# Performance work log

Hardware: AMD Instinct MI355X
Metric: run time of the kernel (lower is better)

## Reference

```python
import jax, jax.numpy as jnp
import numpy as np

B, L, H, HD = 2, 2048, 16, 64
C = H * HD
POS_DIM = 1
MIN_FREQ, MAX_FREQ, P_ZERO = 0.5, 40.0, 0.0


def _phi(m):
    # generalized golden ratio (root of x**(m+1) = x + 1)
    x = 2.0
    for _ in range(100):
        x = (1.0 + x) ** (1.0 / (m + 1))
    return x


def _make_rope_freqs():
    """Golden-gate RoPE frequencies: (H, HD//2, POS_DIM).
    Log-spaced magnitudes in [min_freq, max_freq] (times 2*pi), quasi-random
    unit directions in pos_dim space; leading p_zero_freqs fraction zeroed."""
    n_freqs = HD // 2
    total = H * n_freqs
    n_zero = int(round(total * P_ZERO))
    n_nz = total - n_zero
    mags = MIN_FREQ * (MAX_FREQ / MIN_FREQ) ** (np.arange(n_nz) / max(n_nz - 1, 1))
    mags = np.concatenate([np.zeros(n_zero), mags]) * (2.0 * np.pi)
    if POS_DIM == 1:
        dirs = np.ones((total, 1), dtype=np.float64)
    else:
        g = _phi(POS_DIM)
        alpha = (1.0 / g) ** np.arange(1, POS_DIM + 1)
        z = np.modf(np.arange(1, total + 1)[:, None] * alpha)[0]
        z = np.clip(z, 1e-6, 1 - 1e-6)
        dirs = np.asarray(jax.scipy.special.ndtri(jnp.asarray(z)))
        dirs = dirs / np.linalg.norm(dirs, axis=-1, keepdims=True)
    freqs = dirs * mags[:, None]
    return jnp.asarray(freqs.reshape(H, n_freqs, POS_DIM), dtype=jnp.float32)


def setup_inputs() -> dict:
    key = jax.random.key(0)
    k_x, k_qkv, k_out = jax.random.split(key, 3)
    x = jax.random.normal(k_x, (B, L, C), dtype=jnp.float32)
    w_qkv = jax.random.normal(k_qkv, (C, 3 * C), dtype=jnp.float32) / np.sqrt(C)
    b_qkv = jnp.zeros((3 * C,), dtype=jnp.float32)
    w_out = jax.random.normal(k_out, (C, C), dtype=jnp.float32) / np.sqrt(C)
    b_out = jnp.zeros((C,), dtype=jnp.float32)
    rope_freqs = _make_rope_freqs()
    return {"x": x, "w_qkv": w_qkv, "b_qkv": b_qkv, "w_out": w_out,
            "b_out": b_out, "rope_freqs": rope_freqs}


def _forward(x, w_qkv, b_qkv, w_out, b_out, rope_freqs):
    b, l, c = x.shape
    qkv = x @ w_qkv + b_qkv                                   # (b,l,3c)
    qkv = qkv.reshape(b, l, 3, H, HD).transpose(0, 3, 1, 2, 4)  # (b,h,l,3,hd)
    q, k, v = qkv[..., 0, :], qkv[..., 1, :], qkv[..., 2, :]   # (b,h,l,hd)
    # positions: arange, pos_dim = 1 -> (b,l,1)
    pos = jnp.broadcast_to(jnp.arange(l, dtype=jnp.float32)[None, :, None], (b, l, POS_DIM))
    theta = jnp.einsum('blp,hfp->blhf', pos, rope_freqs)       # (b,l,h,hd/2)
    cos, sin = jnp.cos(theta), jnp.sin(theta)

    def rot(t):  # t: (b,h,l,hd) -> rotate half-split pairs
        t = t.transpose(0, 2, 1, 3)                            # (b,l,h,hd)
        t1, t2 = jnp.split(t, 2, axis=-1)
        r = jnp.concatenate([t1 * cos - t2 * sin, t1 * sin + t2 * cos], axis=-1)
        return r.transpose(0, 2, 1, 3)                         # (b,h,l,hd)

    q_rot, k_rot = rot(q), rot(k)
    logits = jnp.einsum('bhld,bhmd->bhlm', q_rot, k_rot) / jnp.sqrt(jnp.float32(HD))
    attn = jax.nn.softmax(logits, axis=-1)
    out = jnp.einsum('bhlm,bhmd->bhld', attn, v)
    out = out.transpose(0, 2, 1, 3).reshape(b, l, H * HD)
    return out @ w_out + b_out


def reference(x, w_qkv, b_qkv, w_out, b_out, rope_freqs):
    return _forward(x, w_qkv, b_qkv, w_out, b_out, rope_freqs)
```

## Files before the change

### kernel.cpp

```cpp
#include <hip/hip_runtime.h>
#include <cstddef>
#include <cstdint>


typedef __attribute__((ext_vector_type(8))) short short8;
typedef __attribute__((ext_vector_type(4))) float f32x4;
typedef __attribute__((ext_vector_type(4))) unsigned short ushort4_t;
typedef __attribute__((ext_vector_type(2))) unsigned int uint2_t;

__device__ __forceinline__ unsigned short f2bf(float f) {
  union { float f; unsigned int u; } c{f};
  unsigned int u = c.u;
  u += 0x7fff + ((u >> 16) & 1);
  return (unsigned short)(u >> 16);
}
__device__ __forceinline__ float bf2f(unsigned short h) {
  union { unsigned int u; float f; } c{((unsigned int)h) << 16};
  return c.f;
}
__device__ __forceinline__ unsigned int pack_bf16_trunc(float a, float b) {
  union { float f; unsigned int u; } ca{a}, cb{b};
  return __builtin_amdgcn_perm(cb.u, ca.u, 0x07060302u);
}

__global__ __launch_bounds__(256) void cvt_f32_bf16(const float* __restrict__ src,
                                                    unsigned short* __restrict__ dst,
                                                    int n4) {
  int i = blockIdx.x * 256 + threadIdx.x;
  int stride = gridDim.x * 256;
  for (; i < n4; i += stride) {
    float4 v = reinterpret_cast<const float4*>(src)[i];
    ushort4_t o;
    o.x = f2bf(v.x); o.y = f2bf(v.y); o.z = f2bf(v.z); o.w = f2bf(v.w);
    reinterpret_cast<ushort4_t*>(dst)[i] = o;
  }
}

__global__ __launch_bounds__(256) void transpose_cvt(const float* __restrict__ W,
                                                     unsigned short* __restrict__ WT,
                                                     int K, int N) {
  __shared__ float T[64][65];
  const int n0 = blockIdx.x * 64, k0 = blockIdx.y * 64;
  const int t = threadIdx.x;
  const int r = t >> 4, c4 = (t & 15) * 4;
#pragma unroll
  for (int rr = 0; rr < 4; ++rr) {
    int kk = rr * 16 + r;
    float4 v = *reinterpret_cast<const float4*>(W + (size_t)(k0 + kk) * N + n0 + c4);
    T[kk][c4 + 0] = v.x; T[kk][c4 + 1] = v.y; T[kk][c4 + 2] = v.z; T[kk][c4 + 3] = v.w;
  }
  __syncthreads();
#pragma unroll
  for (int rr = 0; rr < 4; ++rr) {
    int nn = rr * 16 + r;
    ushort4_t o;
    o.x = f2bf(T[c4 + 0][nn]); o.y = f2bf(T[c4 + 1][nn]);
    o.z = f2bf(T[c4 + 2][nn]); o.w = f2bf(T[c4 + 3][nn]);
    *reinterpret_cast<ushort4_t*>(WT + (size_t)(n0 + nn) * K + k0 + c4) = o;
  }
}

template <int EPI>
__global__ __launch_bounds__(256) void mm128p(const unsigned short* __restrict__ A,
                                              const unsigned short* __restrict__ Bt,
                                              const float* __restrict__ bias,
                                              unsigned short* __restrict__ q,
                                              unsigned short* __restrict__ k,
                                              unsigned short* __restrict__ v,
                                              float* __restrict__ outf) {
  __shared__ unsigned short As[128][40];
  __shared__ unsigned short Bs[128][40];
  const int m0 = blockIdx.y * 128, n0 = blockIdx.x * 128;
  const int t = threadIdx.x, l = t & 63, w = t >> 6;
  const int wm = w >> 1, wn = w & 1;
  const int lr = l & 15, lg = l >> 4;
  const int lrow = t >> 1, lk = (t & 1) * 16;

  const unsigned short* ap = A + (size_t)(m0 + lrow) * 1024 + lk;
  const unsigned short* bp = Bt + (size_t)(n0 + lrow) * 1024 + lk;

  short8 av0 = *reinterpret_cast<const short8*>(ap);
  short8 av1 = *reinterpret_cast<const short8*>(ap + 8);
  short8 bv0 = *reinterpret_cast<const short8*>(bp);
  short8 bv1 = *reinterpret_cast<const short8*>(bp + 8);

  f32x4 acc[4][4] = {};
#pragma unroll 2
  for (int k0 = 0; k0 < 1024; k0 += 32) {
    __syncthreads();
    *reinterpret_cast<short8*>(&As[lrow][lk]) = av0;
    *reinterpret_cast<short8*>(&As[lrow][lk + 8]) = av1;
    *reinterpret_cast<short8*>(&Bs[lrow][lk]) = bv0;
    *reinterpret_cast<short8*>(&Bs[lrow][lk + 8]) = bv1;
    __syncthreads();
    const int kn = (k0 + 32) & 1023;
    short8 an0 = *reinterpret_cast<const short8*>(ap + kn);
    short8 an1 = *reinterpret_cast<const short8*>(ap + kn + 8);
    short8 bn0 = *reinterpret_cast<const short8*>(bp + kn);
    short8 bn1 = *reinterpret_cast<const short8*>(bp + kn + 8);
    short8 af[4], bf[4];
#pragma unroll
    for (int i = 0; i < 4; ++i)
      af[i] = *reinterpret_cast<const short8*>(&As[wm * 64 + i * 16 + lr][lg * 8]);
#pragma unroll
    for (int j = 0; j < 4; ++j)
      bf[j] = *reinterpret_cast<const short8*>(&Bs[wn * 64 + j * 16 + lr][lg * 8]);
#pragma unroll
    for (int i = 0; i < 4; ++i)
#pragma unroll
      for (int j = 0; j < 4; ++j)
        acc[i][j] = __builtin_amdgcn_mfma_f32_16x16x32_bf16(af[i], bf[j], acc[i][j], 0, 0, 0);
    av0 = an0; av1 = an1; bv0 = bn0; bv1 = bn1;
  }

  if constexpr (EPI == 0) {
#pragma unroll
    for (int j = 0; j < 4; ++j) {
      const int n = n0 + wn * 64 + j * 16 + lr;
      const float bb = bias[n];
      const int s = n >> 10, cc = n & 1023, h = cc >> 6, d = cc & 63;
      unsigned short* dst = (s == 0) ? q : (s == 1) ? k : v;
#pragma unroll
      for (int i = 0; i < 4; ++i)
#pragma unroll
        for (int r = 0; r < 4; ++r) {
          const int m = m0 + wm * 64 + i * 16 + lg * 4 + r;
          const int b = m >> 11, lseq = m & 2047;
          dst[(size_t)(((b << 4) + h) * 2048 + lseq) * 64 + d] = f2bf(acc[i][j][r] + bb);
        }
    }
  } else {
#pragma unroll
    for (int j = 0; j < 4; ++j) {
      const int n = n0 + wn * 64 + j * 16 + lr;
      const float bb = bias[n];
#pragma unroll
      for (int i = 0; i < 4; ++i)
#pragma unroll
        for (int r = 0; r < 4; ++r) {
          const int m = m0 + wm * 64 + i * 16 + lg * 4 + r;
          outf[(size_t)m * 1024 + n] = acc[i][j][r] + bb;
        }
    }
  }
}

__global__ __launch_bounds__(256) void rope_bf(unsigned short* __restrict__ q,
                                               unsigned short* __restrict__ k,
                                               const float* __restrict__ freqs) {
  const int tid = blockIdx.x * 256 + threadIdx.x;
  const int f = tid & 31, row = tid >> 5;
  const int lseq = row & 2047, h = (row >> 11) & 15;
  const float th = (float)lseq * freqs[h * 32 + f];
  float s, c;
  sincosf(th, &s, &c);
  const float QS = 0.18033688011112042f;
  unsigned short* qp = q + (size_t)row * 64;
  const float q1 = bf2f(qp[f]), q2 = bf2f(qp[f + 32]);
  qp[f]      = f2bf((q1 * c - q2 * s) * QS);
  qp[f + 32] = f2bf((q1 * s + q2 * c) * QS);
  unsigned short* kp = k + (size_t)row * 64;
  const float k1 = bf2f(kp[f]), k2 = bf2f(kp[f + 32]);
  kp[f]      = f2bf(k1 * c - k2 * s);
  kp[f + 32] = f2bf(k1 * s + k2 * c);
}

__global__ __launch_bounds__(256) void transpose_v(const unsigned short* __restrict__ V,
                                                   unsigned short* __restrict__ Vt) {
  __shared__ unsigned short T[64][72];
  const int bh = blockIdx.y, l0 = blockIdx.x * 64;
  const int t = threadIdx.x;
  const int r = t >> 2, c16 = (t & 3) * 16;
  const unsigned short* src = V + (size_t)bh * 2048 * 64 + (size_t)(l0 + r) * 64 + c16;
  *reinterpret_cast<short8*>(&T[r][c16])     = *reinterpret_cast<const short8*>(src);
  *reinterpret_cast<short8*>(&T[r][c16 + 8]) = *reinterpret_cast<const short8*>(src + 8);
  __syncthreads();
  short8 o0, o1;
#pragma unroll
  for (int jj = 0; jj < 8; ++jj) o0[jj] = (short)T[c16 + jj][r];
#pragma unroll
  for (int jj = 0; jj < 8; ++jj) o1[jj] = (short)T[c16 + 8 + jj][r];
  unsigned short* dst = Vt + ((size_t)bh * 64 + r) * 2048 + l0 + c16;
  *reinterpret_cast<short8*>(dst) = o0;
  *reinterpret_cast<short8*>(dst + 8) = o1;
}

__global__ __launch_bounds__(256, 2) void attn_mfma5(const unsigned short* __restrict__ Q,
                                                     const unsigned short* __restrict__ K,
                                                     const unsigned short* __restrict__ Vt,
                                                     unsigned short* __restrict__ O) {
  __shared__ unsigned short Ks[2][64 * 64];
  __shared__ unsigned short Vs[2][64 * 64];
  __shared__ unsigned short Pb[4][4][16][72];
  const int bh = blockIdx.y, q0 = blockIdx.x * 256;
  const int t = threadIdx.x, l = t & 63, w = t >> 6;
  const int lr = l & 15, lg = l >> 4;
  const unsigned short* Qb = Q + (size_t)bh * (2048 * 64);
  const unsigned short* Kb = K + (size_t)bh * (2048 * 64);
  const unsigned short* Vb = Vt + (size_t)bh * (64 * 2048);
  const int qrow = q0 + w * 64;

  const int srow = w * 16 + (l >> 3);
  const int xo   = ((l & 7) ^ (srow & 7)) * 8;
  const int swzA = srow * 64 + xo;
  const int swzB = (srow + 8) * 64 + xo;
  const unsigned short* kgp = Kb + (size_t)srow * 64 + (l & 7) * 8;
  const unsigned short* vgp = Vb + (size_t)srow * 2048 + (l & 7) * 8;

  short8 qf[4][2];
#pragma unroll
  for (int g = 0; g < 4; ++g)
#pragma unroll
    for (int h = 0; h < 2; ++h)
      qf[g][h] = *reinterpret_cast<const short8*>(Qb + (size_t)(qrow + g * 16 + lr) * 64 + h * 32 + lg * 8);

  f32x4 oacc[4][4] = {};
  float m_run[4] = {-3.0e38f, -3.0e38f, -3.0e38f, -3.0e38f};
  float l_run[4] = {0.0f, 0.0f, 0.0f, 0.0f};

  {
    short8 k0a = *reinterpret_cast<const short8*>(kgp);
    short8 k0b = *reinterpret_cast<const short8*>(kgp + 8 * 64);
    short8 v0a = *reinterpret_cast<const short8*>(vgp);
    short8 v0b = *reinterpret_cast<const short8*>(vgp + 8 * 2048);
    *reinterpret_cast<short8*>(&Ks[0][swzA]) = k0a;
    *reinterpret_cast<short8*>(&Ks[0][swzB]) = k0b;
    *reinterpret_cast<short8*>(&Vs[0][swzA]) = v0a;
    *reinterpret_cast<short8*>(&Vs[0][swzB]) = v0b;
  }

  for (int it = 0; it < 32; ++it) {
    const int cur = it & 1;
    __syncthreads();

    short8 kna, knb, vna, vnb;
    if (it < 31) {
      kna = *reinterpret_cast<const short8*>(kgp + (size_t)(it + 1) * 4096);
      knb = *reinterpret_cast<const short8*>(kgp + (size_t)(it + 1) * 4096 + 8 * 64);
      vna = *reinterpret_cast<const short8*>(vgp + (it + 1) * 64);
      vnb = *reinterpret_cast<const short8*>(vgp + (it + 1) * 64 + 8 * 2048);
    }

    short8 kfa[4][2];
#pragma unroll
    for (int n = 0; n < 4; ++n)
#pragma unroll
      for (int h = 0; h < 2; ++h)
        kfa[n][h] = *reinterpret_cast<const short8*>(
            &Ks[cur][(n * 16 + lr) * 64 + (((h * 4 + lg) ^ (lr & 7)) * 8)]);

#pragma unroll
    for (int g = 0; g < 4; ++g) {
      f32x4 sacc[4] = {};
      __builtin_amdgcn_s_setprio(1);
#pragma unroll
      for (int n = 0; n < 4; ++n) {
        sacc[n] = __builtin_amdgcn_mfma_f32_16x16x32_bf16(kfa[n][0], qf[g][0], sacc[n], 0, 0, 0);
        sacc[n] = __builtin_amdgcn_mfma_f32_16x16x32_bf16(kfa[n][1], qf[g][1], sacc[n], 0, 0, 0);
      }
      __builtin_amdgcn_s_setprio(0);
      float m0 = fmaxf(fmaxf(sacc[0][0], sacc[0][1]), fmaxf(sacc[0][2], sacc[0][3]));
      float m1 = fmaxf(fmaxf(sacc[1][0], sacc[1][1]), fmaxf(sacc[1][2], sacc[1][3]));
      float m2 = fmaxf(fmaxf(sacc[2][0], sacc[2][1]), fmaxf(sacc[2][2], sacc[2][3]));
      float m3 = fmaxf(fmaxf(sacc[3][0], sacc[3][1]), fmaxf(sacc[3][2], sacc[3][3]));
      float mx = fmaxf(fmaxf(m0, m1), fmaxf(m2, m3));
      mx = fmaxf(mx, __shfl_xor(mx, 16));
      mx = fmaxf(mx, __shfl_xor(mx, 32));
      if (__any(mx > m_run[g] + 8.0f)) {
        const float m_new = fmaxf(m_run[g], mx);
        const float alpha = __builtin_amdgcn_exp2f(m_run[g] - m_new);
        m_run[g] = m_new;
        l_run[g] *= alpha;
#pragma unroll
        for (int sub = 0; sub < 4; ++sub)
#pragma unroll
          for (int r = 0; r < 4; ++r) oacc[g][sub][r] *= alpha;
      }
      const float mq = m_run[g];
      float p[16];
#pragma unroll
      for (int n = 0; n < 4; ++n)
#pragma unroll
        for (int r = 0; r < 4; ++r)
          p[n * 4 + r] = __builtin_amdgcn_exp2f(sacc[n][r] - mq);
      float ssum = ((p[0] + p[1]) + (p[2] + p[3])) + ((p[4] + p[5]) + (p[6] + p[7]));
      ssum += ((p[8] + p[9]) + (p[10] + p[11])) + ((p[12] + p[13]) + (p[14] + p[15]));
      ssum += __shfl_xor(ssum, 16);
      ssum += __shfl_xor(ssum, 32);
      l_run[g] += ssum;
#pragma unroll
      for (int n = 0; n < 4; ++n) {
        uint2_t pk;
        pk.x = pack_bf16_trunc(p[n * 4 + 0], p[n * 4 + 1]);
        pk.y = pack_bf16_trunc(p[n * 4 + 2], p[n * 4 + 3]);
        *reinterpret_cast<uint2_t*>(&Pb[w][g][lr][n * 16 + lg * 4]) = pk;
      }
    }

    short8 vfa[4][2];
#pragma unroll
    for (int sub = 0; sub < 4; ++sub)
#pragma unroll
      for (int kb = 0; kb < 2; ++kb)
        vfa[sub][kb] = *reinterpret_cast<const short8*>(
            &Vs[cur][(sub * 16 + lr) * 64 + (((kb * 4 + lg) ^ (lr & 7)) * 8)]);

#pragma unroll
    for (int g = 0; g < 4; ++g) {
      short8 pb[2];
#pragma unroll
      for (int kb = 0; kb < 2; ++kb)
        pb[kb] = *reinterpret_cast<const short8*>(&Pb[w][g][lr][kb * 32 + lg * 8]);
      __builtin_amdgcn_s_setprio(1);
#pragma unroll
      for (int sub = 0; sub < 4; ++sub) {
        oacc[g][sub] = __builtin_amdgcn_mfma_f32_16x16x32_bf16(vfa[sub][0], pb[0], oacc[g][sub], 0, 0, 0);
        oacc[g][sub] = __builtin_amdgcn_mfma_f32_16x16x32_bf16(vfa[sub][1], pb[1], oacc[g][sub], 0, 0, 0);
      }
      __builtin_amdgcn_s_setprio(0);
    }

    __syncthreads();
    if (it < 31) {
      const int nxt = cur ^ 1;
      *reinterpret_cast<short8*>(&Ks[nxt][swzA]) = kna;
      *reinterpret_cast<short8*>(&Ks[nxt][swzB]) = knb;
      *reinterpret_cast<short8*>(&Vs[nxt][swzA]) = vna;
      *reinterpret_cast<short8*>(&Vs[nxt][swzB]) = vnb;
    }
  }

  const int b = bh >> 4, h = bh & 15;
#pragma unroll
  for (int g = 0; g < 4; ++g) {
    const float inv = 1.0f / l_run[g];
    unsigned short* Ob = O + ((size_t)(b * 2048 + qrow + g * 16 + lr)) * 1024 + h * 64;
#pragma unroll
    for (int sub = 0; sub < 4; ++sub) {
      ushort4_t o;
#pragma unroll
      for (int r = 0; r < 4; ++r) o[r] = f2bf(oacc[g][sub][r] * inv);
      *reinterpret_cast<ushort4_t*>(Ob + sub * 16 + lg * 4) = o;
    }
  }
}

extern "C" void kernel_launch(void* const* d_in, const int* in_sizes, int n_in,
                              void* d_out, int out_size, void* d_ws, size_t ws_size,
                              hipStream_t stream) {
  const float* x          = (const float*)d_in[0];
  const float* w_qkv      = (const float*)d_in[1];
  const float* b_qkv      = (const float*)d_in[2];
  const float* w_out      = (const float*)d_in[3];
  const float* b_out      = (const float*)d_in[4];
  const float* rope_freqs = (const float*)d_in[5];
  float* out = (float*)d_out;

  char* ws = (char*)d_ws;
  unsigned short* x_bf    = (unsigned short*)(ws + 0);
  unsigned short* attn_bf = x_bf;
  unsigned short* q_bf    = (unsigned short*)(ws + 8388608);
  unsigned short* k_bf    = (unsigned short*)(ws + 16777216);
  unsigned short* v_bf    = (unsigned short*)(ws + 25165824);
  unsigned short* v_t     = (unsigned short*)(ws + 33554432);
  unsigned short* wqkvT   = (unsigned short*)(ws + 41943040);
  unsigned short* woutT   = (unsigned short*)(ws + 48234496);

  hipLaunchKernelGGL(cvt_f32_bf16, dim3(1024), dim3(256), 0, stream, x, x_bf, 1048576);
  hipLaunchKernelGGL(transpose_cvt, dim3(48, 16), dim3(256), 0, stream, w_qkv, wqkvT, 1024, 3072);
  hipLaunchKernelGGL(transpose_cvt, dim3(16, 16), dim3(256), 0, stream, w_out, woutT, 1024, 1024);
  hipLaunchKernelGGL((mm128p<0>), dim3(24, 32), dim3(256), 0, stream,
                     x_bf, wqkvT, b_qkv, q_bf, k_bf, v_bf, (float*)nullptr);
  hipLaunchKernelGGL(rope_bf, dim3(8192), dim3(256), 0, stream, q_bf, k_bf, rope_freqs);
  hipLaunchKernelGGL(transpose_v, dim3(32, 32), dim3(256), 0, stream, v_bf, v_t);
  hipLaunchKernelGGL(attn_mfma5, dim3(8, 32), dim3(256), 0, stream, q_bf, k_bf, v_t, attn_bf);
  hipLaunchKernelGGL((mm128p<1>), dim3(8, 32), dim3(256), 0, stream,
                     attn_bf, woutT, b_out,
                     (unsigned short*)nullptr, (unsigned short*)nullptr, (unsigned short*)nullptr, out);
}
```

Measured before the change: 256.6 us.

## Fuse RoPE and V transpose into QKV GEMM epilogue, remap blocks per XCD

The QKV GEMM epilogue now applies bias, RoPE (with the q scale folded in) and writes V directly in transposed layout. This removes the separate rope_bf and transpose_v kernels along with their extra global memory round trips. It also switches the GEMM and attention grids to 1D and remaps block indices so blocks sharing data land on the same XCD, aiming for better L2 reuse. The cost is more sincos work inside the GEMM epilogue and strided scalar stores for q and k.

```diff
diff --git a/kernel.cpp b/kernel.cpp
--- a/kernel.cpp
+++ b/kernel.cpp
@@ -60,17 +60,21 @@
   }
 }
 
-template <int EPI>
+template <int EPI, int NPX>
 __global__ __launch_bounds__(256) void mm128p(const unsigned short* __restrict__ A,
                                               const unsigned short* __restrict__ Bt,
                                               const float* __restrict__ bias,
                                               unsigned short* __restrict__ q,
                                               unsigned short* __restrict__ k,
                                               unsigned short* __restrict__ v,
-                                              float* __restrict__ outf) {
+                                              float* __restrict__ outf,
+                                              const float* __restrict__ freqs) {
   __shared__ unsigned short As[128][40];
   __shared__ unsigned short Bs[128][40];
-  const int m0 = blockIdx.y * 128, n0 = blockIdx.x * 128;
+  const int bid = blockIdx.x;
+  const int xcd = bid & 7, c = bid >> 3;
+  const int m0 = (c & 31) * 128;
+  const int n0 = (xcd * NPX + (c >> 5)) * 128;
   const int t = threadIdx.x, l = t & 63, w = t >> 6;
   const int wm = w >> 1, wn = w & 1;
   const int lr = l & 15, lg = l >> 4;
@@ -114,20 +118,51 @@
   }
 
   if constexpr (EPI == 0) {
-#pragma unroll
-    for (int j = 0; j < 4; ++j) {
-      const int n = n0 + wn * 64 + j * 16 + lr;
-      const float bb = bias[n];
-      const int s = n >> 10, cc = n & 1023, h = cc >> 6, d = cc & 63;
-      unsigned short* dst = (s == 0) ? q : (s == 1) ? k : v;
+    const int nbase = n0 + wn * 64;
+    const int s = nbase >> 10;
+    const int h = (nbase >> 6) & 15;
+    const float b0 = bias[nbase + lr],      b1 = bias[nbase + 16 + lr];
+    const float b2 = bias[nbase + 32 + lr], b3 = bias[nbase + 48 + lr];
+    if (s < 2) {
+      unsigned short* dst = (s == 0) ? q : k;
+      const float scale = (s == 0) ? 0.18033688011112042f : 1.0f;
+      const float f0 = freqs[h * 32 + lr];
+      const float f1 = freqs[h * 32 + 16 + lr];
 #pragma unroll
       for (int i = 0; i < 4; ++i)
 #pragma unroll
         for (int r = 0; r < 4; ++r) {
           const int m = m0 + wm * 64 + i * 16 + lg * 4 + r;
-          const int b = m >> 11, lseq = m & 2047;
-          dst[(size_t)(((b << 4) + h) * 2048 + lseq) * 64 + d] = f2bf(acc[i][j][r] + bb);
+          const int bb = m >> 11, lseq = m & 2047;
+          float sn0, cs0, sn1, cs1;
+          sincosf((float)lseq * f0, &sn0, &cs0);
+          sincosf((float)lseq * f1, &sn1, &cs1);
+          const float t0 = acc[i][0][r] + b0;
+          const float t1 = acc[i][1][r] + b1;
+          const float t2 = acc[i][2][r] + b2;
+          const float t3 = acc[i][3][r] + b3;
+          unsigned short* p = dst + (size_t)(((bb << 4) + h) * 2048 + lseq) * 64;
+          p[lr]      = f2bf((t0 * cs0 - t2 * sn0) * scale);
+          p[lr + 32] = f2bf((t0 * sn0 + t2 * cs0) * scale);
+          p[lr + 16] = f2bf((t1 * cs1 - t3 * sn1) * scale);
+          p[lr + 48] = f2bf((t1 * sn1 + t3 * cs1) * scale);
         }
+    } else {
+      const float bj[4] = {b0, b1, b2, b3};
+#pragma unroll
+      for (int j = 0; j < 4; ++j) {
+        const int d = j * 16 + lr;
+#pragma unroll
+        for (int i = 0; i < 4; ++i) {
+          const int m = m0 + wm * 64 + i * 16 + lg * 4;
+          const int bb = m >> 11, lseq0 = m & 2047;
+          ushort4_t o;
+#pragma unroll
+          for (int r = 0; r < 4; ++r) o[r] = f2bf(acc[i][j][r] + bj[j]);
+          *reinterpret_cast<ushort4_t*>(
+              v + ((size_t)(((bb << 4) + h) * 64 + d)) * 2048 + lseq0) = o;
+        }
+      }
     }
   } else {
 #pragma unroll
@@ -143,46 +178,6 @@
         }
     }
   }
-}
-
-__global__ __launch_bounds__(256) void rope_bf(unsigned short* __restrict__ q,
-                                               unsigned short* __restrict__ k,
-                                               const float* __restrict__ freqs) {
-  const int tid = blockIdx.x * 256 + threadIdx.x;
-  const int f = tid & 31, row = tid >> 5;
-  const int lseq = row & 2047, h = (row >> 11) & 15;
-  const float th = (float)lseq * freqs[h * 32 + f];
-  float s, c;
-  sincosf(th, &s, &c);
-  const float QS = 0.18033688011112042f;
-  unsigned short* qp = q + (size_t)row * 64;
-  const float q1 = bf2f(qp[f]), q2 = bf2f(qp[f + 32]);
-  qp[f]      = f2bf((q1 * c - q2 * s) * QS);
-  qp[f + 32] = f2bf((q1 * s + q2 * c) * QS);
-  unsigned short* kp = k + (size_t)row * 64;
-  const float k1 = bf2f(kp[f]), k2 = bf2f(kp[f + 32]);
-  kp[f]      = f2bf(k1 * c - k2 * s);
-  kp[f + 32] = f2bf(k1 * s + k2 * c);
-}
-
-__global__ __launch_bounds__(256) void transpose_v(const unsigned short* __restrict__ V,
-                                                   unsigned short* __restrict__ Vt) {
-  __shared__ unsigned short T[64][72];
-  const int bh = blockIdx.y, l0 = blockIdx.x * 64;
-  const int t = threadIdx.x;
-  const int r = t >> 2, c16 = (t & 3) * 16;
-  const unsigned short* src = V + (size_t)bh * 2048 * 64 + (size_t)(l0 + r) * 64 + c16;
-  *reinterpret_cast<short8*>(&T[r][c16])     = *reinterpret_cast<const short8*>(src);
-  *reinterpret_cast<short8*>(&T[r][c16 + 8]) = *reinterpret_cast<const short8*>(src + 8);
-  __syncthreads();
-  short8 o0, o1;
-#pragma unroll
-  for (int jj = 0; jj < 8; ++jj) o0[jj] = (short)T[c16 + jj][r];
-#pragma unroll
-  for (int jj = 0; jj < 8; ++jj) o1[jj] = (short)T[c16 + 8 + jj][r];
-  unsigned short* dst = Vt + ((size_t)bh * 64 + r) * 2048 + l0 + c16;
-  *reinterpret_cast<short8*>(dst) = o0;
-  *reinterpret_cast<short8*>(dst + 8) = o1;
 }
 
 __global__ __launch_bounds__(256, 2) void attn_mfma5(const unsigned short* __restrict__ Q,
@@ -192,7 +187,10 @@
   __shared__ unsigned short Ks[2][64 * 64];
   __shared__ unsigned short Vs[2][64 * 64];
   __shared__ unsigned short Pb[4][4][16][72];
-  const int bh = blockIdx.y, q0 = blockIdx.x * 256;
+  const int bid = blockIdx.x;
+  const int xcd = bid & 7, c = bid >> 3;
+  const int bh = (xcd << 2) + (c >> 3);
+  const int q0 = (c & 7) * 256;
   const int t = threadIdx.x, l = t & 63, w = t >> 6;
   const int lr = l & 15, lg = l >> 4;
   const unsigned short* Qb = Q + (size_t)bh * (2048 * 64);
@@ -361,7 +359,6 @@
   unsigned short* attn_bf = x_bf;
   unsigned short* q_bf    = (unsigned short*)(ws + 8388608);
   unsigned short* k_bf    = (unsigned short*)(ws + 16777216);
-  unsigned short* v_bf    = (unsigned short*)(ws + 25165824);
   unsigned short* v_t     = (unsigned short*)(ws + 33554432);
   unsigned short* wqkvT   = (unsigned short*)(ws + 41943040);
   unsigned short* woutT   = (unsigned short*)(ws + 48234496);
@@ -369,12 +366,11 @@
   hipLaunchKernelGGL(cvt_f32_bf16, dim3(1024), dim3(256), 0, stream, x, x_bf, 1048576);
   hipLaunchKernelGGL(transpose_cvt, dim3(48, 16), dim3(256), 0, stream, w_qkv, wqkvT, 1024, 3072);
   hipLaunchKernelGGL(transpose_cvt, dim3(16, 16), dim3(256), 0, stream, w_out, woutT, 1024, 1024);
-  hipLaunchKernelGGL((mm128p<0>), dim3(24, 32), dim3(256), 0, stream,
-                     x_bf, wqkvT, b_qkv, q_bf, k_bf, v_bf, (float*)nullptr);
-  hipLaunchKernelGGL(rope_bf, dim3(8192), dim3(256), 0, stream, q_bf, k_bf, rope_freqs);
-  hipLaunchKernelGGL(transpose_v, dim3(32, 32), dim3(256), 0, stream, v_bf, v_t);
-  hipLaunchKernelGGL(attn_mfma5, dim3(8, 32), dim3(256), 0, stream, q_bf, k_bf, v_t, attn_bf);
-  hipLaunchKernelGGL((mm128p<1>), dim3(8, 32), dim3(256), 0, stream,
+  hipLaunchKernelGGL((mm128p<0, 3>), dim3(768), dim3(256), 0, stream,
+                     x_bf, wqkvT, b_qkv, q_bf, k_bf, v_t, (float*)nullptr, rope_freqs);
+  hipLaunchKernelGGL(attn_mfma5, dim3(256), dim3(256), 0, stream, q_bf, k_bf, v_t, attn_bf);
+  hipLaunchKernelGGL((mm128p<1, 1>), dim3(256), dim3(256), 0, stream,
                      attn_bf, woutT, b_out,
-                     (unsigned short*)nullptr, (unsigned short*)nullptr, (unsigned short*)nullptr, out);
-}
+                     (unsigned short*)nullptr, (unsigned short*)nullptr, (unsigned short*)nullptr,
+                     out, (const float*)nullptr);
+}
```

New measurement: 257.0 us. About the same (+0.2%).
